# Kernel optimization log

Measured on AMD Instinct MI355X. Metric: run time of the kernel, lower is better.

The kernel has to match this reference:

```python
import jax, jax.numpy as jnp
import numpy as np

N_NODES = 50000
N_EDGES = 800000
N_LABEL = 200000
IN_C, HID_C, OUT_C = 128, 128, 64


def setup_inputs() -> dict:
    key = jax.random.key(0)
    ks = jax.random.split(key, 9)
    s = lambda fan_in: 1.0 / np.sqrt(fan_in)
    return {
        "x": jax.random.normal(ks[0], (N_NODES, IN_C), jnp.float32),
        "W1": jax.random.normal(ks[1], (IN_C, HID_C), jnp.float32) * s(IN_C),
        "b1": jnp.zeros((HID_C,), jnp.float32),
        "W2": jax.random.normal(ks[2], (HID_C, HID_C), jnp.float32) * s(HID_C),
        "b2": jnp.zeros((HID_C,), jnp.float32),
        "W3": jax.random.normal(ks[3], (HID_C, OUT_C), jnp.float32) * s(HID_C),
        "b3": jnp.zeros((OUT_C,), jnp.float32),
        "edge_index": jax.random.randint(ks[4], (2, N_EDGES), 0, N_NODES, jnp.int32),
        "edge_label_index": jax.random.randint(ks[5], (2, N_LABEL), 0, N_NODES, jnp.int32),
    }


def _gcn_conv(x, W, b, src, dst, dinv, num_nodes):
    # x @ W then symmetric-normalized scatter-sum over edges (self-loops included in src/dst)
    h = x @ W                                  # [N, out]
    norm = dinv[src] * dinv[dst]               # [E+N]
    msgs = h[src] * norm[:, None]              # [E+N, out]
    out = jax.ops.segment_sum(msgs, dst, num_segments=num_nodes)
    return out + b


def _encode(x, W1, b1, W2, b2, W3, b3, edge_index, num_nodes):
    loops = jnp.arange(num_nodes, dtype=edge_index.dtype)
    src = jnp.concatenate([edge_index[0], loops])
    dst = jnp.concatenate([edge_index[1], loops])
    # degree (with self-loops) at targets; deg >= 1 so rsqrt is safe
    deg = jax.ops.segment_sum(jnp.ones(dst.shape[0], x.dtype), dst, num_segments=num_nodes)
    dinv = jax.lax.rsqrt(deg)
    z = _gcn_conv(x, W1, b1, src, dst, dinv, num_nodes)
    z = jax.nn.relu(z)  # dropout treated as eval-mode identity
    z = _gcn_conv(z, W2, b2, src, dst, dinv, num_nodes)
    z = jax.nn.relu(z)
    z = _gcn_conv(z, W3, b3, src, dst, dinv, num_nodes)
    return z


def reference(x, W1, b1, W2, b2, W3, b3, edge_index, edge_label_index):
    z = _encode(x, W1, b1, W2, b2, W3, b3, edge_index, N_NODES)
    # decode: gather both endpoints, elementwise mul, sum over feature dim
    return (z[edge_label_index[0]] * z[edge_label_index[1]]).sum(axis=-1)
```

## Files before the change

### kernel.cpp

```cpp
#include <hip/hip_runtime.h>

#define N_NODES 50000
#define N_EDGES 800000
#define N_LABEL 200000
#define ROW_BLOCKS 782

typedef __attribute__((ext_vector_type(4))) float f32x4;
typedef _Float16 f16;
typedef __attribute__((ext_vector_type(8))) _Float16 f16x8;

__global__ __launch_bounds__(256)
void k_zero(int4* __restrict__ p, int n4) {
    int i = blockIdx.x * 256 + threadIdx.x;
    if (i < n4) p[i] = int4{0, 0, 0, 0};
}

__global__ __launch_bounds__(256)
void k_prep(const float* __restrict__ W1, const float* __restrict__ W2,
            const float* __restrict__ W3,
            f16* WT1h, f16* WT1l, f16* WT2h, f16* WT2l, f16* WT3h, f16* WT3l,
            const int* __restrict__ dst, int* cnt) {
    int b = blockIdx.x, tid = threadIdx.x;
    if (b < 64) {
        int t = b * 256 + tid;
        int c = t >> 7, k = t & 127;
        float w = W1[k * 128 + c];
        f16 h = (f16)w;
        WT1h[c * 128 + k] = h; WT1l[c * 128 + k] = (f16)(w - (float)h);
        w = W2[k * 128 + c];
        h = (f16)w;
        WT2h[c * 128 + k] = h; WT2l[c * 128 + k] = (f16)(w - (float)h);
        if (c < 64) {
            w = W3[k * 64 + c];
            h = (f16)w;
            WT3h[c * 128 + k] = h; WT3l[c * 128 + k] = (f16)(w - (float)h);
        }
    } else {
        int vb = b - 64;
        int g = vb & 7;
        int i = (vb >> 3) * 256 + tid;
        int d = dst[i];
        if ((unsigned)(d - g * 6250) < 6250u) atomicAdd(&cnt[d], 1);
    }
}

__global__ __launch_bounds__(256)
void k_partial(const int* __restrict__ cnt, float* __restrict__ dinv,
               int* __restrict__ bsum, int N) {
    __shared__ int wsum[4];
    int b = blockIdx.x, t = threadIdx.x;
    int i = b * 256 + t;
    int v = (i < N) ? cnt[i] : 0;
    if (i < N) dinv[i] = rsqrtf((float)v + 1.0f);
    int s = v;
#pragma unroll
    for (int d = 1; d < 64; d <<= 1) s += __shfl_xor(s, d, 64);
    if ((t & 63) == 0) wsum[t >> 6] = s;
    __syncthreads();
    if (t == 0) bsum[b] = wsum[0] + wsum[1] + wsum[2] + wsum[3];
}

__global__ __launch_bounds__(256)
void k_offsets(const int* __restrict__ cnt, const int* __restrict__ bsum,
               int* __restrict__ off, int N, int NB) {
    __shared__ int wsum[4];
    __shared__ int add0_s;
    int b = blockIdx.x, t = threadIdx.x;
    int v0 = (t < b && t < NB) ? bsum[t] : 0;
    int s0 = v0;
#pragma unroll
    for (int d = 1; d < 64; d <<= 1) s0 += __shfl_xor(s0, d, 64);
    if ((t & 63) == 0) wsum[t >> 6] = s0;
    __syncthreads();
    if (t == 0) add0_s = wsum[0] + wsum[1] + wsum[2] + wsum[3];
    __syncthreads();
    int add = add0_s;
    __syncthreads();
    int i = b * 256 + t;
    int v = (i < N) ? cnt[i] : 0;
    int lane = t & 63, w = t >> 6;
    int sv = v;
#pragma unroll
    for (int d = 1; d < 64; d <<= 1) {
        int u = __shfl_up(sv, d, 64);
        if (lane >= d) sv += u;
    }
    if (lane == 63) wsum[w] = sv;
    __syncthreads();
    for (int ww = 0; ww < w; ++ww) add += wsum[ww];
    if (i < N) off[i + 1] = add + sv;
    if (i == 0) off[0] = 0;
}

__global__ __launch_bounds__(256)
void k_bucket(const int* __restrict__ srcv, const int* __restrict__ dstv,
              const int* __restrict__ off, int* cnt2, unsigned short* __restrict__ csr) {
    int vb = blockIdx.x;
    int g = vb & 7;
    int i = (vb >> 3) * 256 + threadIdx.x;
    int d = dstv[i];
    if ((unsigned)(d - g * 6250) < 6250u) {
        int slot = off[d] + atomicAdd(&cnt2[d], 1);
        csr[slot] = (unsigned short)srcv[i];
    }
}

__global__ __launch_bounds__(256)
void k_gemm1(const float* __restrict__ x,
             const f16* __restrict__ WTh, const f16* __restrict__ WTl,
             const float* __restrict__ dinv, f16* __restrict__ A, int N) {
    constexpr int M = 128, NCB = 4;
    __shared__ f16 Hs[64 * 136];
    __shared__ f16 Ls[64 * 136];
    int b = blockIdx.x;
    int c0 = (b & 1) * 64;
    int t = threadIdx.x;

#pragma unroll
    for (int i = 0; i < 4; ++i) {
        int ch = t + i * 256;
        int col = ch >> 4;
        int kc = (ch & 15) * 8;
        *(f16x8*)&Hs[col * 136 + kc] = *(const f16x8*)&WTh[(long)(c0 + col) * 128 + kc];
        *(f16x8*)&Ls[col * 136 + kc] = *(const f16x8*)&WTl[(long)(c0 + col) * 128 + kc];
    }

    int wv = t >> 6, l = t & 63;
    int r0w = (b >> 1) * 64 + wv * 16;
    int arow = r0w + (l & 15);
    if (arow >= N) arow = N - 1;
    int kb = (l >> 4) * 8;

    f16x8 ah[4], al[4];
#pragma unroll
    for (int ks = 0; ks < 4; ++ks) {
        const float* xp = &x[(long)arow * 128 + ks * 32 + kb];
        float4 a0 = *(const float4*)xp;
        float4 a1 = *(const float4*)(xp + 4);
        float fv[8] = {a0.x, a0.y, a0.z, a0.w, a1.x, a1.y, a1.z, a1.w};
#pragma unroll
        for (int j = 0; j < 8; ++j) {
            f16 h = (f16)fv[j];
            ah[ks][j] = h;
            al[ks][j] = (f16)(fv[j] - (float)h);
        }
    }
    __syncthreads();

    f32x4 acc[NCB];
#pragma unroll
    for (int cb = 0; cb < NCB; ++cb) acc[cb] = f32x4{0.f, 0.f, 0.f, 0.f};
#pragma unroll
    for (int ks = 0; ks < 4; ++ks) {
#pragma unroll
        for (int cb = 0; cb < NCB; ++cb) {
            int wi = (cb * 16 + (l & 15)) * 136 + ks * 32 + kb;
            f16x8 bh = *(const f16x8*)&Hs[wi];
            f16x8 bl = *(const f16x8*)&Ls[wi];
            acc[cb] = __builtin_amdgcn_mfma_f32_16x16x32_f16(ah[ks], bh, acc[cb], 0, 0, 0);
            acc[cb] = __builtin_amdgcn_mfma_f32_16x16x32_f16(ah[ks], bl, acc[cb], 0, 0, 0);
            acc[cb] = __builtin_amdgcn_mfma_f32_16x16x32_f16(al[ks], bh, acc[cb], 0, 0, 0);
        }
    }
    int rbase = r0w + (l >> 4) * 4;
    float dv[4];
#pragma unroll
    for (int i = 0; i < 4; ++i) dv[i] = (rbase + i < N) ? dinv[rbase + i] : 0.f;
#pragma unroll
    for (int cb = 0; cb < NCB; ++cb) {
#pragma unroll
        for (int i = 0; i < 4; ++i) {
            int r = rbase + i;
            if (r < N) A[(long)r * M + c0 + cb * 16 + (l & 15)] = (f16)(acc[cb][i] * dv[i]);
        }
    }
}

template<int M>
__global__ __launch_bounds__(256)
void k_gemm23(const f16* __restrict__ B,
              const f16* __restrict__ WTh, const f16* __restrict__ WTl,
              const float* __restrict__ dinv, f16* __restrict__ A, int N) {
    constexpr int NCB = M / 32;
    constexpr int HC = M / 2;
    __shared__ f16 Hs[HC * 136];
    __shared__ f16 Ls[HC * 136];
    int b = blockIdx.x;
    int c0 = (b & 1) * HC;
    int t = threadIdx.x;

#pragma unroll
    for (int i = 0; i < HC / 16; ++i) {
        int ch = t + i * 256;
        int col = ch >> 4;
        int kc = (ch & 15) * 8;
        *(f16x8*)&Hs[col * 136 + kc] = *(const f16x8*)&WTh[(long)(c0 + col) * 128 + kc];
        *(f16x8*)&Ls[col * 136 + kc] = *(const f16x8*)&WTl[(long)(c0 + col) * 128 + kc];
    }

    int wv = t >> 6, l = t & 63;
    int r0w = (b >> 1) * 64 + wv * 16;
    int arow = r0w + (l & 15);
    if (arow >= N) arow = N - 1;
    int kb = (l >> 4) * 8;

    f16x8 a[4];
#pragma unroll
    for (int ks = 0; ks < 4; ++ks)
        a[ks] = *(const f16x8*)&B[(long)arow * 128 + ks * 32 + kb];
    __syncthreads();

    f32x4 acc[NCB];
#pragma unroll
    for (int cb = 0; cb < NCB; ++cb) acc[cb] = f32x4{0.f, 0.f, 0.f, 0.f};
#pragma unroll
    for (int ks = 0; ks < 4; ++ks) {
#pragma unroll
        for (int cb = 0; cb < NCB; ++cb) {
            int wi = (cb * 16 + (l & 15)) * 136 + ks * 32 + kb;
            f16x8 bh = *(const f16x8*)&Hs[wi];
            f16x8 bl = *(const f16x8*)&Ls[wi];
            acc[cb] = __builtin_amdgcn_mfma_f32_16x16x32_f16(a[ks], bh, acc[cb], 0, 0, 0);
            acc[cb] = __builtin_amdgcn_mfma_f32_16x16x32_f16(a[ks], bl, acc[cb], 0, 0, 0);
        }
    }
    int rbase = r0w + (l >> 4) * 4;
    float dv[4];
#pragma unroll
    for (int i = 0; i < 4; ++i) dv[i] = (rbase + i < N) ? dinv[rbase + i] : 0.f;
#pragma unroll
    for (int cb = 0; cb < NCB; ++cb) {
#pragma unroll
        for (int i = 0; i < 4; ++i) {
            int r = rbase + i;
            if (r < N) A[(long)r * M + c0 + cb * 16 + (l & 15)] = (f16)(acc[cb][i] * dv[i]);
        }
    }
}

__global__ __launch_bounds__(256)
void k_gather128(const f16* __restrict__ A, const int* __restrict__ off,
                 const unsigned short* __restrict__ csr, const float* __restrict__ dinv,
                 const float* __restrict__ bias, f16* __restrict__ Bo) {
    int vb = blockIdx.x;
    int g = vb & 7, blk = vb >> 3;
    int t = threadIdx.x;
    int nl = blk * 64 + (t >> 2);
    if (nl >= 25000) return;
    int node = (g & 1) * 25000 + nl;
    int q = (g >> 1) * 32 + (t & 3) * 8;
    const f16* Aq = A + q;

    float acc[8];
    {
        f16x8 v = *(const f16x8*)&Aq[(long)node * 128];
#pragma unroll
        for (int c = 0; c < 8; ++c) acc[c] = (float)v[c];
    }
    int j = off[node], j1 = off[node + 1];
    for (; j + 8 <= j1; j += 8) {
        int s0 = csr[j + 0], s1 = csr[j + 1], s2 = csr[j + 2], s3 = csr[j + 3];
        int s4 = csr[j + 4], s5 = csr[j + 5], s6 = csr[j + 6], s7 = csr[j + 7];
        f16x8 v0 = *(const f16x8*)&Aq[(long)s0 * 128];
        f16x8 v1 = *(const f16x8*)&Aq[(long)s1 * 128];
        f16x8 v2 = *(const f16x8*)&Aq[(long)s2 * 128];
        f16x8 v3 = *(const f16x8*)&Aq[(long)s3 * 128];
        f16x8 v4 = *(const f16x8*)&Aq[(long)s4 * 128];
        f16x8 v5 = *(const f16x8*)&Aq[(long)s5 * 128];
        f16x8 v6 = *(const f16x8*)&Aq[(long)s6 * 128];
        f16x8 v7 = *(const f16x8*)&Aq[(long)s7 * 128];
#pragma unroll
        for (int c = 0; c < 8; ++c)
            acc[c] += ((float)v0[c] + (float)v1[c] + (float)v2[c] + (float)v3[c])
                    + ((float)v4[c] + (float)v5[c] + (float)v6[c] + (float)v7[c]);
    }
    for (; j + 2 <= j1; j += 2) {
        int s0 = csr[j + 0], s1 = csr[j + 1];
        f16x8 v0 = *(const f16x8*)&Aq[(long)s0 * 128];
        f16x8 v1 = *(const f16x8*)&Aq[(long)s1 * 128];
#pragma unroll
        for (int c = 0; c < 8; ++c) acc[c] += (float)v0[c] + (float)v1[c];
    }
    if (j < j1) {
        int s = csr[j];
        f16x8 v = *(const f16x8*)&Aq[(long)s * 128];
#pragma unroll
        for (int c = 0; c < 8; ++c) acc[c] += (float)v[c];
    }
    float sc = dinv[node];
    float4 bb0 = *(const float4*)&bias[q];
    float4 bb1 = *(const float4*)&bias[q + 4];
    float bv[8] = {bb0.x, bb0.y, bb0.z, bb0.w, bb1.x, bb1.y, bb1.z, bb1.w};
    f16x8 o;
#pragma unroll
    for (int c = 0; c < 8; ++c) o[c] = (f16)fmaxf(acc[c] * sc + bv[c], 0.f);
    *(f16x8*)&Bo[(long)node * 128 + q] = o;
}

__global__ __launch_bounds__(256)
void k_gather64(const f16* __restrict__ A, const int* __restrict__ off,
                const unsigned short* __restrict__ csr, const float* __restrict__ dinv,
                const float* __restrict__ bias, float* __restrict__ z) {
    int vb = blockIdx.x;
    int g = vb & 7, blk = vb >> 3;
    int t = threadIdx.x;
    int nl = blk * 64 + (t >> 2);
    if (nl >= 12500) return;
    int node = (g >> 1) * 12500 + nl;
    int q = (g & 1) * 32 + (t & 3) * 8;
    const f16* Aq = A + q;

    float acc[8];
    {
        f16x8 v = *(const f16x8*)&Aq[(long)node * 64];
#pragma unroll
        for (int c = 0; c < 8; ++c) acc[c] = (float)v[c];
    }
    int j = off[node], j1 = off[node + 1];
    for (; j + 8 <= j1; j += 8) {
        int s0 = csr[j + 0], s1 = csr[j + 1], s2 = csr[j + 2], s3 = csr[j + 3];
        int s4 = csr[j + 4], s5 = csr[j + 5], s6 = csr[j + 6], s7 = csr[j + 7];
        f16x8 v0 = *(const f16x8*)&Aq[(long)s0 * 64];
        f16x8 v1 = *(const f16x8*)&Aq[(long)s1 * 64];
        f16x8 v2 = *(const f16x8*)&Aq[(long)s2 * 64];
        f16x8 v3 = *(const f16x8*)&Aq[(long)s3 * 64];
        f16x8 v4 = *(const f16x8*)&Aq[(long)s4 * 64];
        f16x8 v5 = *(const f16x8*)&Aq[(long)s5 * 64];
        f16x8 v6 = *(const f16x8*)&Aq[(long)s6 * 64];
        f16x8 v7 = *(const f16x8*)&Aq[(long)s7 * 64];
#pragma unroll
        for (int c = 0; c < 8; ++c)
            acc[c] += ((float)v0[c] + (float)v1[c] + (float)v2[c] + (float)v3[c])
                    + ((float)v4[c] + (float)v5[c] + (float)v6[c] + (float)v7[c]);
    }
    for (; j + 2 <= j1; j += 2) {
        int s0 = csr[j + 0], s1 = csr[j + 1];
        f16x8 v0 = *(const f16x8*)&Aq[(long)s0 * 64];
        f16x8 v1 = *(const f16x8*)&Aq[(long)s1 * 64];
#pragma unroll
        for (int c = 0; c < 8; ++c) acc[c] += (float)v0[c] + (float)v1[c];
    }
    if (j < j1) {
        int s = csr[j];
        f16x8 v = *(const f16x8*)&Aq[(long)s * 64];
#pragma unroll
        for (int c = 0; c < 8; ++c) acc[c] += (float)v[c];
    }
    float sc = dinv[node];
    float4 bb0 = *(const float4*)&bias[q];
    float4 bb1 = *(const float4*)&bias[q + 4];
    float4 o0, o1;
    o0.x = acc[0] * sc + bb0.x; o0.y = acc[1] * sc + bb0.y;
    o0.z = acc[2] * sc + bb0.z; o0.w = acc[3] * sc + bb0.w;
    o1.x = acc[4] * sc + bb1.x; o1.y = acc[5] * sc + bb1.y;
    o1.z = acc[6] * sc + bb1.z; o1.w = acc[7] * sc + bb1.w;
    *(float4*)&z[(long)node * 64 + q] = o0;
    *(float4*)&z[(long)node * 64 + q + 4] = o1;
}

__global__ __launch_bounds__(256)
void k_decode_part(const float* __restrict__ z, const int* __restrict__ eli,
                   float* __restrict__ P) {
    int vb = blockIdx.x;
    int g = vb & 7, blk = vb >> 3;
    int el = blk * 256 + threadIdx.x;
    if (el >= 100000) return;
    int e = (g & 1) * 100000 + el;
    int cs = g >> 1;
    const float* za = &z[(long)eli[e] * 64 + cs * 16];
    const float* zb = &z[(long)eli[N_LABEL + e] * 64 + cs * 16];
    float s = 0.f;
#pragma unroll
    for (int i = 0; i < 4; ++i) {
        float4 a = *(const float4*)&za[i * 4];
        float4 b = *(const float4*)&zb[i * 4];
        s += a.x * b.x + a.y * b.y + a.z * b.z + a.w * b.w;
    }
    P[cs * N_LABEL + e] = s;
}

__global__ __launch_bounds__(256)
void k_decode_red(const float* __restrict__ P, float* __restrict__ out) {
    int e = blockIdx.x * 256 + threadIdx.x;
    if (e < N_LABEL)
        out[e] = (P[e] + P[N_LABEL + e]) + (P[2 * N_LABEL + e] + P[3 * N_LABEL + e]);
}

extern "C" void kernel_launch(void* const* d_in, const int* in_sizes, int n_in,
                              void* d_out, int out_size, void* d_ws, size_t ws_size,
                              hipStream_t stream) {
    const float* x   = (const float*)d_in[0];
    const float* W1  = (const float*)d_in[1];
    const float* b1  = (const float*)d_in[2];
    const float* W2  = (const float*)d_in[3];
    const float* b2  = (const float*)d_in[4];
    const float* W3  = (const float*)d_in[5];
    const float* b3  = (const float*)d_in[6];
    const int*   ei  = (const int*)d_in[7];
    const int*   eli = (const int*)d_in[8];
    float* out = (float*)d_out;

    char* ws = (char*)d_ws;
    float* dinv = (float*)ws;                  ws += 50048 * 4;
    f16*   A    = (f16*)ws;                    ws += (long)N_NODES * 128 * 2;
    f16*   B    = (f16*)ws;                    ws += (long)N_NODES * 128 * 2;
    float* z    = (float*)ws;                  ws += (long)N_NODES * 64 * 4;
    float* P    = (float*)ws;                  ws += (long)4 * N_LABEL * 4;
    int*   cnt  = (int*)ws;                    ws += 50048 * 4;
    int*   cnt2 = (int*)ws;                    ws += 50048 * 4;
    int*   off  = (int*)ws;                    ws += 50048 * 4;
    unsigned short* csr = (unsigned short*)ws; ws += (long)N_EDGES * 2;
    int*   bsum = (int*)ws;                    ws += 256 * 4;
    f16*   WT1h = (f16*)ws;                    ws += 16384 * 2;
    f16*   WT1l = (f16*)ws;                    ws += 16384 * 2;
    f16*   WT2h = (f16*)ws;                    ws += 16384 * 2;
    f16*   WT2l = (f16*)ws;                    ws += 16384 * 2;
    f16*   WT3h = (f16*)ws;                    ws += 8192 * 2;
    f16*   WT3l = (f16*)ws;                    ws += 8192 * 2;

    const int* esrc = ei;
    const int* edst = ei + N_EDGES;

    const int NB = (N_NODES + 255) / 256;

    k_zero   <<<98, 256, 0, stream>>>((int4*)cnt, 25024);
    k_prep   <<<25064, 256, 0, stream>>>(W1, W2, W3, WT1h, WT1l, WT2h, WT2l,
                                         WT3h, WT3l, edst, cnt);
    k_partial<<<NB, 256, 0, stream>>>(cnt, dinv, bsum, N_NODES);
    k_offsets<<<NB, 256, 0, stream>>>(cnt, bsum, off, N_NODES, NB);
    k_bucket <<<25000, 256, 0, stream>>>(esrc, edst, off, cnt2, csr);

    k_gemm1<<<ROW_BLOCKS * 2, 256, 0, stream>>>(x, WT1h, WT1l, dinv, A, N_NODES);
    k_gather128<<<391 * 8, 256, 0, stream>>>(A, off, csr, dinv, b1, B);
    k_gemm23<128><<<ROW_BLOCKS * 2, 256, 0, stream>>>(B, WT2h, WT2l, dinv, A, N_NODES);
    k_gather128<<<391 * 8, 256, 0, stream>>>(A, off, csr, dinv, b2, B);
    k_gemm23<64><<<ROW_BLOCKS * 2, 256, 0, stream>>>(B, WT3h, WT3l, dinv, A, N_NODES);
    k_gather64<<<196 * 8, 256, 0, stream>>>(A, off, csr, dinv, b3, z);

    k_decode_part<<<391 * 8, 256, 0, stream>>>(z, eli, P);
    k_decode_red <<<(N_LABEL + 255) / 256, 256, 0, stream>>>(P, out);
}
```

Measured before the change: 247.3 us.

## Store node features in 32-channel slabs and fuse decode into one kernel

```diff
diff --git a/kernel.cpp b/kernel.cpp
--- a/kernel.cpp
+++ b/kernel.cpp
@@ -8,6 +8,7 @@
 typedef __attribute__((ext_vector_type(4))) float f32x4;
 typedef _Float16 f16;
 typedef __attribute__((ext_vector_type(8))) _Float16 f16x8;
+
 
 __global__ __launch_bounds__(256)
 void k_zero(int4* __restrict__ p, int n4) {
@@ -108,8 +109,8 @@
 __global__ __launch_bounds__(256)
 void k_gemm1(const float* __restrict__ x,
              const f16* __restrict__ WTh, const f16* __restrict__ WTl,
-             const float* __restrict__ dinv, f16* __restrict__ A, int N) {
-    constexpr int M = 128, NCB = 4;
+             const float* __restrict__ dinv, f16* __restrict__ As, int N) {
+    constexpr int NCB = 4;
     __shared__ f16 Hs[64 * 136];
     __shared__ f16 Ls[64 * 136];
     int b = blockIdx.x;
@@ -168,19 +169,21 @@
     for (int i = 0; i < 4; ++i) dv[i] = (rbase + i < N) ? dinv[rbase + i] : 0.f;
 #pragma unroll
     for (int cb = 0; cb < NCB; ++cb) {
+        int fc = c0 + cb * 16 + (l & 15);
+        long sb = (long)(fc >> 5) * N_NODES * 32 + (fc & 31);
 #pragma unroll
         for (int i = 0; i < 4; ++i) {
             int r = rbase + i;
-            if (r < N) A[(long)r * M + c0 + cb * 16 + (l & 15)] = (f16)(acc[cb][i] * dv[i]);
+            if (r < N) As[sb + (long)r * 32] = (f16)(acc[cb][i] * dv[i]);
         }
     }
 }
 
 template<int M>
 __global__ __launch_bounds__(256)
-void k_gemm23(const f16* __restrict__ B,
+void k_gemm23(const f16* __restrict__ Bs,
               const f16* __restrict__ WTh, const f16* __restrict__ WTl,
-              const float* __restrict__ dinv, f16* __restrict__ A, int N) {
+              const float* __restrict__ dinv, f16* __restrict__ As, int N) {
     constexpr int NCB = M / 32;
     constexpr int HC = M / 2;
     __shared__ f16 Hs[HC * 136];
@@ -207,7 +210,7 @@
     f16x8 a[4];
 #pragma unroll
     for (int ks = 0; ks < 4; ++ks)
-        a[ks] = *(const f16x8*)&B[(long)arow * 128 + ks * 32 + kb];
+        a[ks] = *(const f16x8*)&Bs[((long)ks * N_NODES + arow) * 32 + kb];
     __syncthreads();
 
     f32x4 acc[NCB];
@@ -230,30 +233,33 @@
     for (int i = 0; i < 4; ++i) dv[i] = (rbase + i < N) ? dinv[rbase + i] : 0.f;
 #pragma unroll
     for (int cb = 0; cb < NCB; ++cb) {
+        int fc = c0 + cb * 16 + (l & 15);
+        long sb = (long)(fc >> 5) * N_NODES * 32 + (fc & 31);
 #pragma unroll
         for (int i = 0; i < 4; ++i) {
             int r = rbase + i;
-            if (r < N) A[(long)r * M + c0 + cb * 16 + (l & 15)] = (f16)(acc[cb][i] * dv[i]);
-        }
-    }
-}
-
-__global__ __launch_bounds__(256)
-void k_gather128(const f16* __restrict__ A, const int* __restrict__ off,
+            if (r < N) As[sb + (long)r * 32] = (f16)(acc[cb][i] * dv[i]);
+        }
+    }
+}
+
+__global__ __launch_bounds__(256)
+void k_gather128(const f16* __restrict__ As, const int* __restrict__ off,
                  const unsigned short* __restrict__ csr, const float* __restrict__ dinv,
-                 const float* __restrict__ bias, f16* __restrict__ Bo) {
+                 const float* __restrict__ bias, f16* __restrict__ Bs) {
     int vb = blockIdx.x;
     int g = vb & 7, blk = vb >> 3;
     int t = threadIdx.x;
     int nl = blk * 64 + (t >> 2);
     if (nl >= 25000) return;
     int node = (g & 1) * 25000 + nl;
-    int q = (g >> 1) * 32 + (t & 3) * 8;
-    const f16* Aq = A + q;
+    int cs = g >> 1;
+    int qq = (t & 3) * 8;
+    const f16* Aq = As + (long)cs * N_NODES * 32 + qq;
 
     float acc[8];
     {
-        f16x8 v = *(const f16x8*)&Aq[(long)node * 128];
+        f16x8 v = *(const f16x8*)&Aq[(long)node * 32];
 #pragma unroll
         for (int c = 0; c < 8; ++c) acc[c] = (float)v[c];
     }
@@ -261,14 +267,14 @@
     for (; j + 8 <= j1; j += 8) {
         int s0 = csr[j + 0], s1 = csr[j + 1], s2 = csr[j + 2], s3 = csr[j + 3];
         int s4 = csr[j + 4], s5 = csr[j + 5], s6 = csr[j + 6], s7 = csr[j + 7];
-        f16x8 v0 = *(const f16x8*)&Aq[(long)s0 * 128];
-        f16x8 v1 = *(const f16x8*)&Aq[(long)s1 * 128];
-        f16x8 v2 = *(const f16x8*)&Aq[(long)s2 * 128];
-        f16x8 v3 = *(const f16x8*)&Aq[(long)s3 * 128];
-        f16x8 v4 = *(const f16x8*)&Aq[(long)s4 * 128];
-        f16x8 v5 = *(const f16x8*)&Aq[(long)s5 * 128];
-        f16x8 v6 = *(const f16x8*)&Aq[(long)s6 * 128];
-        f16x8 v7 = *(const f16x8*)&Aq[(long)s7 * 128];
+        f16x8 v0 = *(const f16x8*)&Aq[(long)s0 * 32];
+        f16x8 v1 = *(const f16x8*)&Aq[(long)s1 * 32];
+        f16x8 v2 = *(const f16x8*)&Aq[(long)s2 * 32];
+        f16x8 v3 = *(const f16x8*)&Aq[(long)s3 * 32];
+        f16x8 v4 = *(const f16x8*)&Aq[(long)s4 * 32];
+        f16x8 v5 = *(const f16x8*)&Aq[(long)s5 * 32];
+        f16x8 v6 = *(const f16x8*)&Aq[(long)s6 * 32];
+        f16x8 v7 = *(const f16x8*)&Aq[(long)s7 * 32];
 #pragma unroll
         for (int c = 0; c < 8; ++c)
             acc[c] += ((float)v0[c] + (float)v1[c] + (float)v2[c] + (float)v3[c])
@@ -276,29 +282,30 @@
     }
     for (; j + 2 <= j1; j += 2) {
         int s0 = csr[j + 0], s1 = csr[j + 1];
-        f16x8 v0 = *(const f16x8*)&Aq[(long)s0 * 128];
-        f16x8 v1 = *(const f16x8*)&Aq[(long)s1 * 128];
+        f16x8 v0 = *(const f16x8*)&Aq[(long)s0 * 32];
+        f16x8 v1 = *(const f16x8*)&Aq[(long)s1 * 32];
 #pragma unroll
         for (int c = 0; c < 8; ++c) acc[c] += (float)v0[c] + (float)v1[c];
     }
     if (j < j1) {
         int s = csr[j];
-        f16x8 v = *(const f16x8*)&Aq[(long)s * 128];
+        f16x8 v = *(const f16x8*)&Aq[(long)s * 32];
 #pragma unroll
         for (int c = 0; c < 8; ++c) acc[c] += (float)v[c];
     }
     float sc = dinv[node];
+    int q = cs * 32 + qq;
     float4 bb0 = *(const float4*)&bias[q];
     float4 bb1 = *(const float4*)&bias[q + 4];
     float bv[8] = {bb0.x, bb0.y, bb0.z, bb0.w, bb1.x, bb1.y, bb1.z, bb1.w};
     f16x8 o;
 #pragma unroll
     for (int c = 0; c < 8; ++c) o[c] = (f16)fmaxf(acc[c] * sc + bv[c], 0.f);
-    *(f16x8*)&Bo[(long)node * 128 + q] = o;
-}
-
-__global__ __launch_bounds__(256)
-void k_gather64(const f16* __restrict__ A, const int* __restrict__ off,
+    *(f16x8*)&Bs[((long)cs * N_NODES + node) * 32 + qq] = o;
+}
+
+__global__ __launch_bounds__(256)
+void k_gather64(const f16* __restrict__ As, const int* __restrict__ off,
                 const unsigned short* __restrict__ csr, const float* __restrict__ dinv,
                 const float* __restrict__ bias, float* __restrict__ z) {
     int vb = blockIdx.x;
@@ -307,12 +314,13 @@
     int nl = blk * 64 + (t >> 2);
     if (nl >= 12500) return;
     int node = (g >> 1) * 12500 + nl;
-    int q = (g & 1) * 32 + (t & 3) * 8;
-    const f16* Aq = A + q;
+    int cs = g & 1;
+    int qq = (t & 3) * 8;
+    const f16* Aq = As + (long)cs * N_NODES * 32 + qq;
 
     float acc[8];
     {
-        f16x8 v = *(const f16x8*)&Aq[(long)node * 64];
+        f16x8 v = *(const f16x8*)&Aq[(long)node * 32];
 #pragma unroll
         for (int c = 0; c < 8; ++c) acc[c] = (float)v[c];
     }
@@ -320,14 +328,14 @@
     for (; j + 8 <= j1; j += 8) {
         int s0 = csr[j + 0], s1 = csr[j + 1], s2 = csr[j + 2], s3 = csr[j + 3];
         int s4 = csr[j + 4], s5 = csr[j + 5], s6 = csr[j + 6], s7 = csr[j + 7];
-        f16x8 v0 = *(const f16x8*)&Aq[(long)s0 * 64];
-        f16x8 v1 = *(const f16x8*)&Aq[(long)s1 * 64];
-        f16x8 v2 = *(const f16x8*)&Aq[(long)s2 * 64];
-        f16x8 v3 = *(const f16x8*)&Aq[(long)s3 * 64];
-        f16x8 v4 = *(const f16x8*)&Aq[(long)s4 * 64];
-        f16x8 v5 = *(const f16x8*)&Aq[(long)s5 * 64];
-        f16x8 v6 = *(const f16x8*)&Aq[(long)s6 * 64];
-        f16x8 v7 = *(const f16x8*)&Aq[(long)s7 * 64];
+        f16x8 v0 = *(const f16x8*)&Aq[(long)s0 * 32];
+        f16x8 v1 = *(const f16x8*)&Aq[(long)s1 * 32];
+        f16x8 v2 = *(const f16x8*)&Aq[(long)s2 * 32];
+        f16x8 v3 = *(const f16x8*)&Aq[(long)s3 * 32];
+        f16x8 v4 = *(const f16x8*)&Aq[(long)s4 * 32];
+        f16x8 v5 = *(const f16x8*)&Aq[(long)s5 * 32];
+        f16x8 v6 = *(const f16x8*)&Aq[(long)s6 * 32];
+        f16x8 v7 = *(const f16x8*)&Aq[(long)s7 * 32];
 #pragma unroll
         for (int c = 0; c < 8; ++c)
             acc[c] += ((float)v0[c] + (float)v1[c] + (float)v2[c] + (float)v3[c])
@@ -335,18 +343,19 @@
     }
     for (; j + 2 <= j1; j += 2) {
         int s0 = csr[j + 0], s1 = csr[j + 1];
-        f16x8 v0 = *(const f16x8*)&Aq[(long)s0 * 64];
-        f16x8 v1 = *(const f16x8*)&Aq[(long)s1 * 64];
+        f16x8 v0 = *(const f16x8*)&Aq[(long)s0 * 32];
+        f16x8 v1 = *(const f16x8*)&Aq[(long)s1 * 32];
 #pragma unroll
         for (int c = 0; c < 8; ++c) acc[c] += (float)v0[c] + (float)v1[c];
     }
     if (j < j1) {
         int s = csr[j];
-        f16x8 v = *(const f16x8*)&Aq[(long)s * 64];
+        f16x8 v = *(const f16x8*)&Aq[(long)s * 32];
 #pragma unroll
         for (int c = 0; c < 8; ++c) acc[c] += (float)v[c];
     }
     float sc = dinv[node];
+    int q = cs * 32 + qq;
     float4 bb0 = *(const float4*)&bias[q];
     float4 bb1 = *(const float4*)&bias[q + 4];
     float4 o0, o1;
@@ -358,32 +367,21 @@
     *(float4*)&z[(long)node * 64 + q + 4] = o1;
 }
 
-__global__ __launch_bounds__(256)
-void k_decode_part(const float* __restrict__ z, const int* __restrict__ eli,
-                   float* __restrict__ P) {
-    int vb = blockIdx.x;
-    int g = vb & 7, blk = vb >> 3;
-    int el = blk * 256 + threadIdx.x;
-    if (el >= 100000) return;
-    int e = (g & 1) * 100000 + el;
-    int cs = g >> 1;
-    const float* za = &z[(long)eli[e] * 64 + cs * 16];
-    const float* zb = &z[(long)eli[N_LABEL + e] * 64 + cs * 16];
-    float s = 0.f;
-#pragma unroll
-    for (int i = 0; i < 4; ++i) {
-        float4 a = *(const float4*)&za[i * 4];
-        float4 b = *(const float4*)&zb[i * 4];
-        s += a.x * b.x + a.y * b.y + a.z * b.z + a.w * b.w;
-    }
-    P[cs * N_LABEL + e] = s;
-}
-
-__global__ __launch_bounds__(256)
-void k_decode_red(const float* __restrict__ P, float* __restrict__ out) {
-    int e = blockIdx.x * 256 + threadIdx.x;
-    if (e < N_LABEL)
-        out[e] = (P[e] + P[N_LABEL + e]) + (P[2 * N_LABEL + e] + P[3 * N_LABEL + e]);
+__global__ void k_decode(const float* __restrict__ z, const int* __restrict__ eli,
+                         float* __restrict__ out, int L) {
+    int t = blockIdx.x * blockDim.x + threadIdx.x;
+    int e = t >> 4;
+    int lane = t & 15;
+    if (e >= L) return;
+    int a = eli[e], b = eli[L + e];
+    float4 va = *(const float4*)&z[(long)a * 64 + lane * 4];
+    float4 vb = *(const float4*)&z[(long)b * 64 + lane * 4];
+    float s = va.x * vb.x + va.y * vb.y + va.z * vb.z + va.w * vb.w;
+    s += __shfl_xor(s, 1, 16);
+    s += __shfl_xor(s, 2, 16);
+    s += __shfl_xor(s, 4, 16);
+    s += __shfl_xor(s, 8, 16);
+    if (lane == 0) out[e] = s;
 }
 
 extern "C" void kernel_launch(void* const* d_in, const int* in_sizes, int n_in,
@@ -405,7 +403,6 @@
     f16*   A    = (f16*)ws;                    ws += (long)N_NODES * 128 * 2;
     f16*   B    = (f16*)ws;                    ws += (long)N_NODES * 128 * 2;
     float* z    = (float*)ws;                  ws += (long)N_NODES * 64 * 4;
-    float* P    = (float*)ws;                  ws += (long)4 * N_LABEL * 4;
     int*   cnt  = (int*)ws;                    ws += 50048 * 4;
     int*   cnt2 = (int*)ws;                    ws += 50048 * 4;
     int*   off  = (int*)ws;                    ws += 50048 * 4;
@@ -437,6 +434,5 @@
     k_gemm23<64><<<ROW_BLOCKS * 2, 256, 0, stream>>>(B, WT3h, WT3l, dinv, A, N_NODES);
     k_gather64<<<196 * 8, 256, 0, stream>>>(A, off, csr, dinv, b3, z);
 
-    k_decode_part<<<391 * 8, 256, 0, stream>>>(z, eli, P);
-    k_decode_red <<<(N_LABEL + 255) / 256, 256, 0, stream>>>(P, out);
-}
+    k_decode<<<(N_LABEL * 16 + 255) / 256, 256, 0, stream>>>(z, eli, out, N_LABEL);
+}
```

Measured after the change: 209.8 us. -15.1%, faster.
